# Kernel optimization log

Measured on AMD Instinct MI355X. Metric: run time of the kernel, lower is better.

Reference implementation:

```python
import jax, jax.numpy as jnp
import numpy as np

IN_C = 512
OUT_C = 1024
N = 8192


def _xavier(key, shape):
    fan_in, fan_out = shape[1], shape[0]
    limit = float(np.sqrt(6.0 / (fan_in + fan_out)))
    return jax.random.uniform(key, shape, jnp.float32, -limit, limit)


def setup_inputs() -> dict:
    key = jax.random.key(0)
    ks = jax.random.split(key, 20)
    inp = {
        'x': jax.random.normal(ks[0], (IN_C, N), jnp.float32),
        'c_prev_dim0': jax.random.normal(ks[1], (OUT_C, N), jnp.float32),
        'h_prev_dim0': jax.random.normal(ks[2], (OUT_C, N), jnp.float32),
        'c_prev_dim1': jax.random.normal(ks[3], (OUT_C, N), jnp.float32),
        'h_prev_dim1': jax.random.normal(ks[4], (OUT_C, N), jnp.float32),
    }
    names_x = ['w_ii', 'w_if', 'w_ig', 'w_io']
    names_h = ['w_hi', 'w_hf', 'w_hg', 'w_ho']
    names_b = ['b_i', 'b_f', 'b_g', 'b_o']
    k = 5
    for n in names_x:
        inp[n] = _xavier(ks[k], (OUT_C, IN_C)); k += 1
    for n in names_h:
        inp[n] = _xavier(ks[k], (OUT_C, OUT_C)); k += 1
    for n in names_b:
        inp[n] = _xavier(ks[k], (OUT_C, 1)); k += 1
    inp['weighted_sum'] = jax.random.uniform(ks[k], (2,), jnp.float32)
    return inp


def reference(x, c_prev_dim0, h_prev_dim0, c_prev_dim1, h_prev_dim1,
              w_ii, w_if, w_ig, w_io,
              w_hi, w_hf, w_hg, w_ho,
              b_i, b_f, b_g, b_o,
              weighted_sum):
    # Input projections shared by both spatial directions: (out, N)
    xi = w_ii @ x
    xf = w_if @ x
    xg = w_ig @ x
    xo = w_io @ x

    def gates(h_prev, c_prev):
        i = jax.nn.sigmoid(xi + w_hi @ h_prev + b_i)
        f = jax.nn.sigmoid(xf + w_hf @ h_prev + b_f)
        g = jnp.tanh(xg + w_hg @ h_prev + b_g)
        o = jax.nn.sigmoid(xo + w_ho @ h_prev + b_o)
        c = f * c_prev + i * g
        h = o * jnp.tanh(c)
        return c, h

    ct0, ht0 = gates(h_prev_dim0, c_prev_dim0)
    ct1, ht1 = gates(h_prev_dim1, c_prev_dim1)
    ct = ct0 * weighted_sum[0] + ct1 * weighted_sum[1]
    ht = ht0 * weighted_sum[0] + ht1 * weighted_sum[1]
    return ct, ht
```

## Files before the change

### kernel.cpp

```cpp
#include <hip/hip_runtime.h>
#include <cstdint>
#include <cstddef>

#define IN_C  512
#define OUT_C 1024
#define NSAMP 8192

typedef __bf16 bf16x8 __attribute__((ext_vector_type(8)));
typedef float  f32x4  __attribute__((ext_vector_type(4)));

#define VMCNT(N)  asm volatile("s_waitcnt vmcnt(" #N ")" ::: "memory")
#define BARRIER() asm volatile("s_barrier" ::: "memory")

__device__ __forceinline__ unsigned short f2bf(float f) {
    unsigned int u = __float_as_uint(f);
    u += 0x7FFFu + ((u >> 16) & 1u);
    return (unsigned short)(u >> 16);
}

__device__ __forceinline__ float sigmoid_f(float x) {
    return 1.0f / (1.0f + __expf(-x));
}
__device__ __forceinline__ float tanh_f(float x) {
    float e = __expf(2.0f * x);
    return 1.0f - 2.0f / (e + 1.0f);
}

__global__ void tcvt_kernel(const float* __restrict__ in, unsigned short* __restrict__ out,
                            int R, int C) {
    __shared__ float t[32][33];
    const int tx = threadIdx.x;
    const int ty = threadIdx.y;
    const int c0 = blockIdx.x * 32;
    const int r0 = blockIdx.y * 32;
#pragma unroll
    for (int i = 0; i < 4; ++i)
        t[ty + i * 8][tx] = in[(size_t)(r0 + ty + i * 8) * C + (c0 + tx)];
    __syncthreads();
#pragma unroll
    for (int i = 0; i < 4; ++i)
        out[(size_t)(c0 + ty + i * 8) * R + (r0 + tx)] = f2bf(t[tx][ty + i * 8]);
}

__global__ void cvt_kernel(const float* __restrict__ in, unsigned short* __restrict__ out, int n4) {
    int idx = blockIdx.x * blockDim.x + threadIdx.x;
    if (idx < n4) {
        float4 v = reinterpret_cast<const float4*>(in)[idx];
        ushort4 o;
        o.x = f2bf(v.x); o.y = f2bf(v.y); o.z = f2bf(v.z); o.w = f2bf(v.w);
        reinterpret_cast<ushort4*>(out)[idx] = o;
    }
}

template<int G0, int G1, int ND>
__device__ __forceinline__ void mfma_phase(f32x4 (&acc)[2][4][2][2],
                                           const bf16x8 (&aF0)[2],
                                           const bf16x8 (&aF1)[2],
                                           const bf16x8 (&bF)[2][2]) {
    __builtin_amdgcn_s_setprio(1);
#pragma unroll
    for (int d = 0; d < ND; ++d)
#pragma unroll
        for (int fm = 0; fm < 2; ++fm)
#pragma unroll
            for (int fn = 0; fn < 2; ++fn) {
                acc[d][G0][fm][fn] = __builtin_amdgcn_mfma_f32_16x16x32_bf16(
                    aF0[fm], bF[d][fn], acc[d][G0][fm][fn], 0, 0, 0);
                acc[d][G1][fm][fn] = __builtin_amdgcn_mfma_f32_16x16x32_bf16(
                    aF1[fm], bF[d][fn], acc[d][G1][fm][fn], 0, 0, 0);
            }
    __builtin_amdgcn_s_setprio(0);
}

__global__ __launch_bounds__(512, 2) void mdlstm_main(
    const unsigned short* __restrict__ xT,
    const unsigned short* __restrict__ h0T,
    const unsigned short* __restrict__ h1T,
    const unsigned short* __restrict__ wx,
    const unsigned short* __restrict__ wh,
    const float* __restrict__ b_i, const float* __restrict__ b_f,
    const float* __restrict__ b_g, const float* __restrict__ b_o,
    const float* __restrict__ cp0, const float* __restrict__ cp1,
    const float* __restrict__ wsum,
    float* __restrict__ out)
{
    __shared__ __align__(16) unsigned char smem[131072];

    const int tid  = threadIdx.x;
    const int lane = tid & 63;
    const int wid  = tid >> 6;
    const int wm   = wid >> 2;
    const int wn   = wid & 3;
    const int g4   = lane >> 4;
    const int l16  = lane & 15;

    const int brow = blockIdx.y * 64;
    const int bcol = blockIdx.x * 128;

    const int s_off16 = tid * 16;

    f32x4 acc[2][4][2][2];
#pragma unroll
    for (int d = 0; d < 2; ++d)
#pragma unroll
        for (int q = 0; q < 4; ++q)
#pragma unroll
            for (int a = 0; a < 2; ++a)
#pragma unroll
                for (int b = 0; b < 2; ++b)
                    acc[d][q][a][b] = (f32x4){0.f, 0.f, 0.f, 0.f};

    auto stage_A_half = [&](int buf, int h, const unsigned short* w, int pitchE, int k0) {
#pragma unroll
        for (int i = 0; i < 2; ++i) {
            const int u   = i * 8192 + s_off16;
            const int q   = u >> 12;
            const int v   = u & 4095;
            const int row = v >> 6;
            const int kb  = v & 63;
            const char* src = (const char*)w
                + ((size_t)q * OUT_C * pitchE + (size_t)(brow + row) * pitchE + k0 + h * 32) * 2
                + (kb ^ ((((row >> 1) & 3)) << 4));
            __builtin_amdgcn_global_load_lds((const unsigned int*)src,
                (unsigned int*)(smem + buf * 65536 + h * 32768 + i * 8192 + s_off16), 16, 0, 0);
        }
    };
    auto stage_B_half = [&](int buf, int h, int d, const unsigned short* hT, int pitchE, int k0) {
        const int row = s_off16 >> 6;
        const int kb  = s_off16 & 63;
        const char* src = (const char*)hT
            + ((size_t)(bcol + row) * pitchE + k0 + h * 32) * 2
            + (kb ^ ((((row >> 1) & 3)) << 4));
        __builtin_amdgcn_global_load_lds((const unsigned int*)src,
            (unsigned int*)(smem + buf * 65536 + h * 32768 + 16384 + d * 8192 + s_off16), 16, 0, 0);
    };

    auto fragA = [&](int buf, int h, int q, int fm) -> bf16x8 {
        const int row = wm * 32 + fm * 16 + l16;
        const int off = buf * 65536 + h * 32768 + q * 4096 + row * 64
                        + ((g4 * 16) ^ ((((row >> 1) & 3)) << 4));
        return *reinterpret_cast<const bf16x8*>(smem + off);
    };
    auto fragB = [&](int buf, int h, int d, int fn) -> bf16x8 {
        const int row = wn * 32 + fn * 16 + l16;
        const int off = buf * 65536 + h * 32768 + 16384 + d * 8192 + row * 64
                        + ((g4 * 16) ^ ((((row >> 1) & 3)) << 4));
        return *reinterpret_cast<const bf16x8*>(smem + off);
    };

    bf16x8 aF0[2], aF1[2];
    bf16x8 bF[2][2];

    stage_A_half(0, 0, wx, IN_C, 0);
    stage_B_half(0, 0, 0, xT, IN_C, 0);
    stage_A_half(0, 1, wx, IN_C, 0);
    stage_B_half(0, 1, 0, xT, IN_C, 0);
    VMCNT(3);
    BARRIER();

    for (int st = 0; st < 8; ++st) {
        const int cur = st & 1, nxt = cur ^ 1;
        const bool last = (st == 7);
        const int k0n = last ? 0 : (st + 1) * 64;

#pragma unroll
        for (int fn = 0; fn < 2; ++fn) bF[0][fn] = fragB(cur, 0, 0, fn);
#pragma unroll
        for (int fm = 0; fm < 2; ++fm) { aF0[fm] = fragA(cur, 0, 0, fm); aF1[fm] = fragA(cur, 0, 1, fm); }
        if (!last) stage_A_half(nxt, 0, wx, IN_C, k0n);
        else       stage_A_half(nxt, 0, wh, OUT_C, 0);
        BARRIER();
        mfma_phase<0, 1, 1>(acc, aF0, aF1, bF);
        BARRIER();

#pragma unroll
        for (int fm = 0; fm < 2; ++fm) { aF0[fm] = fragA(cur, 0, 2, fm); aF1[fm] = fragA(cur, 0, 3, fm); }
        if (!last) { stage_B_half(nxt, 0, 0, xT, IN_C, k0n); }
        else       { stage_B_half(nxt, 0, 0, h0T, OUT_C, 0); stage_B_half(nxt, 0, 1, h1T, OUT_C, 0); }
        BARRIER();
        mfma_phase<2, 3, 1>(acc, aF0, aF1, bF);
        if (!last) { VMCNT(3); } else { VMCNT(4); }
        BARRIER();

#pragma unroll
        for (int fn = 0; fn < 2; ++fn) bF[0][fn] = fragB(cur, 1, 0, fn);
#pragma unroll
        for (int fm = 0; fm < 2; ++fm) { aF0[fm] = fragA(cur, 1, 0, fm); aF1[fm] = fragA(cur, 1, 1, fm); }
        if (!last) stage_A_half(nxt, 1, wx, IN_C, k0n);
        else       stage_A_half(nxt, 1, wh, OUT_C, 0);
        BARRIER();
        mfma_phase<0, 1, 1>(acc, aF0, aF1, bF);
        BARRIER();

#pragma unroll
        for (int fm = 0; fm < 2; ++fm) { aF0[fm] = fragA(cur, 1, 2, fm); aF1[fm] = fragA(cur, 1, 3, fm); }
        if (!last) { stage_B_half(nxt, 1, 0, xT, IN_C, k0n); }
        else       { stage_B_half(nxt, 1, 0, h0T, OUT_C, 0); stage_B_half(nxt, 1, 1, h1T, OUT_C, 0); }
        BARRIER();
        mfma_phase<2, 3, 1>(acc, aF0, aF1, bF);
        if (!last) { VMCNT(3); } else { VMCNT(4); }
        BARRIER();
    }

#pragma unroll
    for (int q = 0; q < 4; ++q)
#pragma unroll
        for (int a = 0; a < 2; ++a)
#pragma unroll
            for (int b = 0; b < 2; ++b)
                acc[1][q][a][b] = acc[0][q][a][b];

    for (int st = 0; st < 16; ++st) {
        const int cur = st & 1, nxt = cur ^ 1;
        const bool last = (st == 15);
        const int k0n = last ? 0 : (st + 1) * 64;

#pragma unroll
        for (int d = 0; d < 2; ++d)
#pragma unroll
            for (int fn = 0; fn < 2; ++fn) bF[d][fn] = fragB(cur, 0, d, fn);
#pragma unroll
        for (int fm = 0; fm < 2; ++fm) { aF0[fm] = fragA(cur, 0, 0, fm); aF1[fm] = fragA(cur, 0, 1, fm); }
        if (!last) stage_A_half(nxt, 0, wh, OUT_C, k0n);
        BARRIER();
        mfma_phase<0, 1, 2>(acc, aF0, aF1, bF);
        BARRIER();

#pragma unroll
        for (int fm = 0; fm < 2; ++fm) { aF0[fm] = fragA(cur, 0, 2, fm); aF1[fm] = fragA(cur, 0, 3, fm); }
        if (!last) { stage_B_half(nxt, 0, 0, h0T, OUT_C, k0n); stage_B_half(nxt, 0, 1, h1T, OUT_C, k0n); }
        BARRIER();
        mfma_phase<2, 3, 2>(acc, aF0, aF1, bF);
        if (!last) { VMCNT(4); } else { VMCNT(0); }
        BARRIER();

#pragma unroll
        for (int d = 0; d < 2; ++d)
#pragma unroll
            for (int fn = 0; fn < 2; ++fn) bF[d][fn] = fragB(cur, 1, d, fn);
#pragma unroll
        for (int fm = 0; fm < 2; ++fm) { aF0[fm] = fragA(cur, 1, 0, fm); aF1[fm] = fragA(cur, 1, 1, fm); }
        if (!last) stage_A_half(nxt, 1, wh, OUT_C, k0n);
        BARRIER();
        mfma_phase<0, 1, 2>(acc, aF0, aF1, bF);
        BARRIER();

#pragma unroll
        for (int fm = 0; fm < 2; ++fm) { aF0[fm] = fragA(cur, 1, 2, fm); aF1[fm] = fragA(cur, 1, 3, fm); }
        if (!last) { stage_B_half(nxt, 1, 0, h0T, OUT_C, k0n); stage_B_half(nxt, 1, 1, h1T, OUT_C, k0n); }
        BARRIER();
        mfma_phase<2, 3, 2>(acc, aF0, aF1, bF);
        if (!last) { VMCNT(4); BARRIER(); }
    }

    const float w0 = wsum[0], w1 = wsum[1];
#pragma unroll
    for (int fm = 0; fm < 2; ++fm)
#pragma unroll
        for (int fn = 0; fn < 2; ++fn)
#pragma unroll
            for (int r = 0; r < 4; ++r) {
                const int m = brow + wm * 32 + fm * 16 + g4 * 4 + r;
                const int n = bcol + wn * 32 + fn * 16 + l16;
                const size_t idx = (size_t)m * NSAMP + n;
                const float bi = b_i[m], bff = b_f[m], bg = b_g[m], bo = b_o[m];

                float c0v, h0v, c1v, h1v;
                {
                    float i_ = sigmoid_f(acc[0][0][fm][fn][r] + bi);
                    float f_ = sigmoid_f(acc[0][1][fm][fn][r] + bff);
                    float g_ = tanh_f   (acc[0][2][fm][fn][r] + bg);
                    float o_ = sigmoid_f(acc[0][3][fm][fn][r] + bo);
                    float c_ = f_ * cp0[idx] + i_ * g_;
                    c0v = c_;
                    h0v = o_ * tanh_f(c_);
                }
                {
                    float i_ = sigmoid_f(acc[1][0][fm][fn][r] + bi);
                    float f_ = sigmoid_f(acc[1][1][fm][fn][r] + bff);
                    float g_ = tanh_f   (acc[1][2][fm][fn][r] + bg);
                    float o_ = sigmoid_f(acc[1][3][fm][fn][r] + bo);
                    float c_ = f_ * cp1[idx] + i_ * g_;
                    c1v = c_;
                    h1v = o_ * tanh_f(c_);
                }
                out[idx] = w0 * c0v + w1 * c1v;
                out[(size_t)OUT_C * NSAMP + idx] = w0 * h0v + w1 * h1v;
            }
}

extern "C" void kernel_launch(void* const* d_in, const int* in_sizes, int n_in,
                              void* d_out, int out_size, void* d_ws, size_t ws_size,
                              hipStream_t stream) {
    (void)in_sizes; (void)n_in; (void)out_size; (void)ws_size;

    const float* x    = (const float*)d_in[0];
    const float* cp0  = (const float*)d_in[1];
    const float* hp0  = (const float*)d_in[2];
    const float* cp1  = (const float*)d_in[3];
    const float* hp1  = (const float*)d_in[4];
    const float* wxp[4] = {(const float*)d_in[5], (const float*)d_in[6],
                           (const float*)d_in[7], (const float*)d_in[8]};
    const float* whp[4] = {(const float*)d_in[9], (const float*)d_in[10],
                           (const float*)d_in[11], (const float*)d_in[12]};
    const float* b_i  = (const float*)d_in[13];
    const float* b_f  = (const float*)d_in[14];
    const float* b_g  = (const float*)d_in[15];
    const float* b_o  = (const float*)d_in[16];
    const float* wsum = (const float*)d_in[17];
    float* out = (float*)d_out;

    char* ws = (char*)d_ws;
    unsigned short* xT  = (unsigned short*)(ws);
    unsigned short* h0T = (unsigned short*)(ws + (size_t)8  * 1024 * 1024);
    unsigned short* h1T = (unsigned short*)(ws + (size_t)24 * 1024 * 1024);
    unsigned short* wxc = (unsigned short*)(ws + (size_t)40 * 1024 * 1024);
    unsigned short* whc = (unsigned short*)(ws + (size_t)44 * 1024 * 1024);

    dim3 tb(32, 8);
    tcvt_kernel<<<dim3(NSAMP / 32, IN_C  / 32), tb, 0, stream>>>(x,   xT,  IN_C,  NSAMP);
    tcvt_kernel<<<dim3(NSAMP / 32, OUT_C / 32), tb, 0, stream>>>(hp0, h0T, OUT_C, NSAMP);
    tcvt_kernel<<<dim3(NSAMP / 32, OUT_C / 32), tb, 0, stream>>>(hp1, h1T, OUT_C, NSAMP);

    for (int q = 0; q < 4; ++q)
        cvt_kernel<<<(OUT_C * IN_C / 4) / 256, 256, 0, stream>>>(
            wxp[q], wxc + (size_t)q * OUT_C * IN_C, OUT_C * IN_C / 4);
    for (int q = 0; q < 4; ++q)
        cvt_kernel<<<(OUT_C * OUT_C / 4) / 256, 256, 0, stream>>>(
            whp[q], whc + (size_t)q * OUT_C * OUT_C, OUT_C * OUT_C / 4);

    mdlstm_main<<<dim3(NSAMP / 128, OUT_C / 64), 512, 0, stream>>>(
        xT, h0T, h1T, wxc, whc, b_i, b_f, b_g, b_o, cp0, cp1, wsum, out);
}
```

Measured before the change: 247.6 us.

## Deepen global-to-LDS pipeline to four 32-wide K slots, three in flight

```diff
diff --git a/kernel.cpp b/kernel.cpp
--- a/kernel.cpp
+++ b/kernel.cpp
@@ -9,8 +9,18 @@
 typedef __bf16 bf16x8 __attribute__((ext_vector_type(8)));
 typedef float  f32x4  __attribute__((ext_vector_type(4)));
 
-#define VMCNT(N)  asm volatile("s_waitcnt vmcnt(" #N ")" ::: "memory")
-#define BARRIER() asm volatile("s_barrier" ::: "memory")
+#define SBAR()       __builtin_amdgcn_s_barrier()
+#define SFENCE()     __builtin_amdgcn_sched_barrier(0)
+#define VMCNT_RAW(N) asm volatile("s_waitcnt vmcnt(" #N ")")
+
+__device__ __forceinline__ void wait_vm(int wsel) {
+    SFENCE();
+    if (wsel == 8)      VMCNT_RAW(8);
+    else if (wsel == 6) VMCNT_RAW(6);
+    else if (wsel == 4) VMCNT_RAW(4);
+    else                VMCNT_RAW(0);
+    SFENCE();
+}
 
 __device__ __forceinline__ unsigned short f2bf(float f) {
     unsigned int u = __float_as_uint(f);
@@ -97,8 +107,6 @@
     const int brow = blockIdx.y * 64;
     const int bcol = blockIdx.x * 128;
 
-    const int s_off16 = tid * 16;
-
     f32x4 acc[2][4][2][2];
 #pragma unroll
     for (int d = 0; d < 2; ++d)
@@ -110,97 +118,113 @@
                 for (int b = 0; b < 2; ++b)
                     acc[d][q][a][b] = (f32x4){0.f, 0.f, 0.f, 0.f};
 
-    auto stage_A_half = [&](int buf, int h, const unsigned short* w, int pitchE, int k0) {
-#pragma unroll
-        for (int i = 0; i < 2; ++i) {
-            const int u   = i * 8192 + s_off16;
+    auto stage_A = [&](int slot, const unsigned short* w, int pitchE, int koff) {
+#pragma unroll
+        for (int j = 0; j < 2; ++j) {
+            const int u   = j * 8192 + tid * 16;
             const int q   = u >> 12;
             const int v   = u & 4095;
             const int row = v >> 6;
             const int kb  = v & 63;
             const char* src = (const char*)w
-                + ((size_t)q * OUT_C * pitchE + (size_t)(brow + row) * pitchE + k0 + h * 32) * 2
-                + (kb ^ ((((row >> 1) & 3)) << 4));
+                + ((size_t)q * OUT_C * pitchE + (size_t)(brow + row) * pitchE + koff) * 2
+                + (kb ^ (((row >> 1) & 3) << 4));
             __builtin_amdgcn_global_load_lds((const unsigned int*)src,
-                (unsigned int*)(smem + buf * 65536 + h * 32768 + i * 8192 + s_off16), 16, 0, 0);
+                (unsigned int*)(smem + slot * 32768 + u), 16, 0, 0);
         }
     };
-    auto stage_B_half = [&](int buf, int h, int d, const unsigned short* hT, int pitchE, int k0) {
-        const int row = s_off16 >> 6;
-        const int kb  = s_off16 & 63;
+    auto stage_B = [&](int slot, int d, const unsigned short* hT, int pitchE, int koff) {
+        const int u   = tid * 16;
+        const int row = u >> 6;
+        const int kb  = u & 63;
         const char* src = (const char*)hT
-            + ((size_t)(bcol + row) * pitchE + k0 + h * 32) * 2
-            + (kb ^ ((((row >> 1) & 3)) << 4));
+            + ((size_t)(bcol + row) * pitchE + koff) * 2
+            + (kb ^ (((row >> 1) & 3) << 4));
         __builtin_amdgcn_global_load_lds((const unsigned int*)src,
-            (unsigned int*)(smem + buf * 65536 + h * 32768 + 16384 + d * 8192 + s_off16), 16, 0, 0);
-    };
-
-    auto fragA = [&](int buf, int h, int q, int fm) -> bf16x8 {
+            (unsigned int*)(smem + slot * 32768 + 16384 + d * 8192 + u), 16, 0, 0);
+    };
+
+    auto stage_for = [&](int t, int part) {
+        if (t >= 48) return;
+        if (t < 16) {
+            const int koff = (t >> 1) * 64 + (t & 1) * 32;
+            if (part == 0) stage_A(t & 3, wx, IN_C, koff);
+            else           stage_B(t & 3, 0, xT, IN_C, koff);
+        } else {
+            const int u = t - 16;
+            const int koff = (u >> 1) * 64 + (u & 1) * 32;
+            if (part == 0) stage_A(t & 3, wh, OUT_C, koff);
+            else { stage_B(t & 3, 0, h0T, OUT_C, koff);
+                   stage_B(t & 3, 1, h1T, OUT_C, koff); }
+        }
+    };
+
+    auto fragA = [&](int slot, int q, int fm) -> bf16x8 {
         const int row = wm * 32 + fm * 16 + l16;
-        const int off = buf * 65536 + h * 32768 + q * 4096 + row * 64
-                        + ((g4 * 16) ^ ((((row >> 1) & 3)) << 4));
+        const int off = slot * 32768 + q * 4096 + row * 64
+                        + ((g4 * 16) ^ (((row >> 1) & 3) << 4));
         return *reinterpret_cast<const bf16x8*>(smem + off);
     };
-    auto fragB = [&](int buf, int h, int d, int fn) -> bf16x8 {
+    auto fragB = [&](int slot, int d, int fn) -> bf16x8 {
         const int row = wn * 32 + fn * 16 + l16;
-        const int off = buf * 65536 + h * 32768 + 16384 + d * 8192 + row * 64
-                        + ((g4 * 16) ^ ((((row >> 1) & 3)) << 4));
+        const int off = slot * 32768 + 16384 + d * 8192 + row * 64
+                        + ((g4 * 16) ^ (((row >> 1) & 3) << 4));
         return *reinterpret_cast<const bf16x8*>(smem + off);
     };
 
     bf16x8 aF0[2], aF1[2];
     bf16x8 bF[2][2];
 
-    stage_A_half(0, 0, wx, IN_C, 0);
-    stage_B_half(0, 0, 0, xT, IN_C, 0);
-    stage_A_half(0, 1, wx, IN_C, 0);
-    stage_B_half(0, 1, 0, xT, IN_C, 0);
-    VMCNT(3);
-    BARRIER();
-
-    for (int st = 0; st < 8; ++st) {
-        const int cur = st & 1, nxt = cur ^ 1;
-        const bool last = (st == 7);
-        const int k0n = last ? 0 : (st + 1) * 64;
-
-#pragma unroll
-        for (int fn = 0; fn < 2; ++fn) bF[0][fn] = fragB(cur, 0, 0, fn);
-#pragma unroll
-        for (int fm = 0; fm < 2; ++fm) { aF0[fm] = fragA(cur, 0, 0, fm); aF1[fm] = fragA(cur, 0, 1, fm); }
-        if (!last) stage_A_half(nxt, 0, wx, IN_C, k0n);
-        else       stage_A_half(nxt, 0, wh, OUT_C, 0);
-        BARRIER();
+    auto xhalf = [&](int i, int wsel) {
+        const int slot = i & 3;
+        const int t = i + 3;
+#pragma unroll
+        for (int fn = 0; fn < 2; ++fn) bF[0][fn] = fragB(slot, 0, fn);
+#pragma unroll
+        for (int fm = 0; fm < 2; ++fm) { aF0[fm] = fragA(slot, 0, fm); aF1[fm] = fragA(slot, 1, fm); }
+        stage_for(t, 0);
+        SFENCE(); SBAR(); SFENCE();
         mfma_phase<0, 1, 1>(acc, aF0, aF1, bF);
-        BARRIER();
-
-#pragma unroll
-        for (int fm = 0; fm < 2; ++fm) { aF0[fm] = fragA(cur, 0, 2, fm); aF1[fm] = fragA(cur, 0, 3, fm); }
-        if (!last) { stage_B_half(nxt, 0, 0, xT, IN_C, k0n); }
-        else       { stage_B_half(nxt, 0, 0, h0T, OUT_C, 0); stage_B_half(nxt, 0, 1, h1T, OUT_C, 0); }
-        BARRIER();
+        SFENCE(); SBAR(); SFENCE();
+#pragma unroll
+        for (int fm = 0; fm < 2; ++fm) { aF0[fm] = fragA(slot, 2, fm); aF1[fm] = fragA(slot, 3, fm); }
+        stage_for(t, 1);
+        SFENCE(); SBAR(); SFENCE();
         mfma_phase<2, 3, 1>(acc, aF0, aF1, bF);
-        if (!last) { VMCNT(3); } else { VMCNT(4); }
-        BARRIER();
-
-#pragma unroll
-        for (int fn = 0; fn < 2; ++fn) bF[0][fn] = fragB(cur, 1, 0, fn);
-#pragma unroll
-        for (int fm = 0; fm < 2; ++fm) { aF0[fm] = fragA(cur, 1, 0, fm); aF1[fm] = fragA(cur, 1, 1, fm); }
-        if (!last) stage_A_half(nxt, 1, wx, IN_C, k0n);
-        else       stage_A_half(nxt, 1, wh, OUT_C, 0);
-        BARRIER();
-        mfma_phase<0, 1, 1>(acc, aF0, aF1, bF);
-        BARRIER();
-
-#pragma unroll
-        for (int fm = 0; fm < 2; ++fm) { aF0[fm] = fragA(cur, 1, 2, fm); aF1[fm] = fragA(cur, 1, 3, fm); }
-        if (!last) { stage_B_half(nxt, 1, 0, xT, IN_C, k0n); }
-        else       { stage_B_half(nxt, 1, 0, h0T, OUT_C, 0); stage_B_half(nxt, 1, 1, h1T, OUT_C, 0); }
-        BARRIER();
-        mfma_phase<2, 3, 1>(acc, aF0, aF1, bF);
-        if (!last) { VMCNT(3); } else { VMCNT(4); }
-        BARRIER();
-    }
+        wait_vm(wsel);
+        SBAR(); SFENCE();
+    };
+
+    auto hhalf = [&](int i, int wsel, bool stg) {
+        const int slot = i & 3;
+        const int t = stg ? (i + 3) : 48;
+#pragma unroll
+        for (int d = 0; d < 2; ++d)
+#pragma unroll
+            for (int fn = 0; fn < 2; ++fn) bF[d][fn] = fragB(slot, d, fn);
+#pragma unroll
+        for (int fm = 0; fm < 2; ++fm) { aF0[fm] = fragA(slot, 0, fm); aF1[fm] = fragA(slot, 1, fm); }
+        stage_for(t, 0);
+        SFENCE(); SBAR(); SFENCE();
+        mfma_phase<0, 1, 2>(acc, aF0, aF1, bF);
+        SFENCE(); SBAR(); SFENCE();
+#pragma unroll
+        for (int fm = 0; fm < 2; ++fm) { aF0[fm] = fragA(slot, 2, fm); aF1[fm] = fragA(slot, 3, fm); }
+        stage_for(t, 1);
+        SFENCE(); SBAR(); SFENCE();
+        mfma_phase<2, 3, 2>(acc, aF0, aF1, bF);
+        wait_vm(wsel);
+        SBAR(); SFENCE();
+    };
+
+    stage_for(0, 0); stage_for(0, 1);
+    stage_for(1, 0); stage_for(1, 1);
+    stage_for(2, 0); stage_for(2, 1);
+    wait_vm(6);
+    SBAR(); SFENCE();
+
+    for (int i = 0; i < 15; ++i) xhalf(i, 6);
+    xhalf(15, 8);
 
 #pragma unroll
     for (int q = 0; q < 4; ++q)
@@ -210,48 +234,10 @@
             for (int b = 0; b < 2; ++b)
                 acc[1][q][a][b] = acc[0][q][a][b];
 
-    for (int st = 0; st < 16; ++st) {
-        const int cur = st & 1, nxt = cur ^ 1;
-        const bool last = (st == 15);
-        const int k0n = last ? 0 : (st + 1) * 64;
-
-#pragma unroll
-        for (int d = 0; d < 2; ++d)
-#pragma unroll
-            for (int fn = 0; fn < 2; ++fn) bF[d][fn] = fragB(cur, 0, d, fn);
-#pragma unroll
-        for (int fm = 0; fm < 2; ++fm) { aF0[fm] = fragA(cur, 0, 0, fm); aF1[fm] = fragA(cur, 0, 1, fm); }
-        if (!last) stage_A_half(nxt, 0, wh, OUT_C, k0n);
-        BARRIER();
-        mfma_phase<0, 1, 2>(acc, aF0, aF1, bF);
-        BARRIER();
-
-#pragma unroll
-        for (int fm = 0; fm < 2; ++fm) { aF0[fm] = fragA(cur, 0, 2, fm); aF1[fm] = fragA(cur, 0, 3, fm); }
-        if (!last) { stage_B_half(nxt, 0, 0, h0T, OUT_C, k0n); stage_B_half(nxt, 0, 1, h1T, OUT_C, k0n); }
-        BARRIER();
-        mfma_phase<2, 3, 2>(acc, aF0, aF1, bF);
-        if (!last) { VMCNT(4); } else { VMCNT(0); }
-        BARRIER();
-
-#pragma unroll
-        for (int d = 0; d < 2; ++d)
-#pragma unroll
-            for (int fn = 0; fn < 2; ++fn) bF[d][fn] = fragB(cur, 1, d, fn);
-#pragma unroll
-        for (int fm = 0; fm < 2; ++fm) { aF0[fm] = fragA(cur, 1, 0, fm); aF1[fm] = fragA(cur, 1, 1, fm); }
-        if (!last) stage_A_half(nxt, 1, wh, OUT_C, k0n);
-        BARRIER();
-        mfma_phase<0, 1, 2>(acc, aF0, aF1, bF);
-        BARRIER();
-
-#pragma unroll
-        for (int fm = 0; fm < 2; ++fm) { aF0[fm] = fragA(cur, 1, 2, fm); aF1[fm] = fragA(cur, 1, 3, fm); }
-        if (!last) { stage_B_half(nxt, 1, 0, h0T, OUT_C, k0n); stage_B_half(nxt, 1, 1, h1T, OUT_C, k0n); }
-        BARRIER();
-        mfma_phase<2, 3, 2>(acc, aF0, aF1, bF);
-        if (!last) { VMCNT(4); BARRIER(); }
-    }
+    for (int i = 16; i <= 44; ++i) hhalf(i, 8, true);
+    hhalf(45, 4, false);
+    hhalf(46, 0, false);
+    hhalf(47, 0, false);
 
     const float w0 = wsum[0], w1 = wsum[1];
 #pragma unroll
```

After: 252.6 us. +2.0%, slower.
